# Kernel optimization log

Measured on AMD Instinct MI355X. Metric: run time of the kernel, lower is better.

Reference implementation:

```python
import jax, jax.numpy as jnp
import numpy as np

B, H, S, D = 2, 8, 2048, 64
N_HASHES = 6
EPS = 1e-8


def setup_inputs() -> dict:
    key = jax.random.key(0)
    kq, kk, kv, kr = jax.random.split(key, 4)
    Q = jax.random.normal(kq, (B, H, S, D), dtype=jnp.float32)
    K = jax.random.normal(kk, (B, H, S, D), dtype=jnp.float32)
    V = jax.random.normal(kv, (B, H, S, D), dtype=jnp.float32)
    rotations = jax.random.normal(kr, (H, N_HASHES, D), dtype=jnp.float32)
    return {"Q": Q, "K": K, "V": V, "rotations": rotations}


def _buckets(X, rotations, powers):
    # X: [b,h,l,d] -> integer bucket id per position, [b,h,l]
    Xn = X / (jnp.linalg.norm(X, axis=-1, keepdims=True) + 1e-8)
    bits = jnp.einsum('bhld,hnd->bhln', Xn, rotations) > 0
    return jnp.sum(bits.astype(jnp.int32) * powers, axis=-1)


def reference(Q, K, V, rotations):
    n_hashes = rotations.shape[1]
    d = Q.shape[-1]
    powers = (2 ** jnp.arange(n_hashes)).astype(jnp.int32)
    q_buckets = _buckets(Q, rotations, powers)  # [b,h,sq]
    k_buckets = _buckets(K, rotations, powers)  # [b,h,sk]
    # queries only attend to keys whose full hash code matches exactly
    match = q_buckets[..., :, None] == k_buckets[..., None, :]  # [b,h,sq,sk]
    scores = jnp.einsum('bhqd,bhkd->bhqk', Q, K) / (d ** 0.5)
    row_has = jnp.any(match, axis=-1, keepdims=True)
    masked = jnp.where(match, scores, -jnp.inf)
    m = jnp.max(masked, axis=-1, keepdims=True)
    m = jnp.where(row_has, m, 0.0)  # avoid -inf for empty rows
    e = jnp.where(match, jnp.exp(scores - m), 0.0)
    weights = e / (jnp.sum(e, axis=-1, keepdims=True) + EPS)
    out = jnp.einsum('bhqk,bhkd->bhqd', weights, V)
    return out / n_hashes
```

## Files before the change

kernel.cpp:

```cpp
#include <hip/hip_runtime.h>
#include <math.h>


constexpr int S_LEN = 2048;
constexpr int D = 64;
constexpr int NHASH = 6;
constexpr int BH = 16;
constexpr int NB = 64;
constexpr int QPAD = 4;
constexpr int PADQ = S_LEN + (QPAD - 1) * NB;
constexpr int NGRP = PADQ / QPAD;
constexpr int KCH = 32;

__global__ __launch_bounds__(256) void lsh_buckets2(const float* __restrict__ Q,
                                                    const float* __restrict__ K,
                                                    const float* __restrict__ rot,
                                                    int* __restrict__ qb,
                                                    int* __restrict__ kb) {
    const int gw   = (blockIdx.x * 256 + threadIdx.x) >> 6;
    const int lane = threadIdx.x & 63;
    const bool isK = gw >= BH * S_LEN;
    const int wid  = isK ? gw - BH * S_LEN : gw;
    const float* X = isK ? K : Q;
    int* dst       = isK ? kb : qb;
    const int h    = (wid >> 11) & 7;

    const float x  = X[(size_t)wid * D + lane];
    const float* r = rot + (size_t)h * NHASH * D + lane;
    float p0 = x * r[0 * D], p1 = x * r[1 * D], p2 = x * r[2 * D];
    float p3 = x * r[3 * D], p4 = x * r[4 * D], p5 = x * r[5 * D];
#pragma unroll
    for (int off = 32; off >= 1; off >>= 1) {
        p0 += __shfl_xor(p0, off, 64);
        p1 += __shfl_xor(p1, off, 64);
        p2 += __shfl_xor(p2, off, 64);
        p3 += __shfl_xor(p3, off, 64);
        p4 += __shfl_xor(p4, off, 64);
        p5 += __shfl_xor(p5, off, 64);
    }
    int bucket = (p0 > 0.f ? 1 : 0) | (p1 > 0.f ? 2 : 0) | (p2 > 0.f ? 4 : 0) |
                 (p3 > 0.f ? 8 : 0) | (p4 > 0.f ? 16 : 0) | (p5 > 0.f ? 32 : 0);
    if (lane == 0) dst[wid] = bucket;
}

__global__ __launch_bounds__(256) void lsh_build_desc(const int* __restrict__ qbuckets,
                                                      const int* __restrict__ kbuckets,
                                                      int* __restrict__ k_list,
                                                      int4* __restrict__ desc_q,
                                                      int* __restrict__ desc_k) {
    __shared__ unsigned short hist[256][NB + 1];
    __shared__ int base[NB + 1];
    __shared__ int seg[NB][4];
    __shared__ int qlist[PADQ];
    __shared__ int kcnt[NB], kst[NB];
    const int which = blockIdx.x >> 4;
    const int bh    = blockIdx.x & 15;
    const int tid   = threadIdx.x;
    const int* src  = (which ? kbuckets : qbuckets) + bh * S_LEN;

    for (int b = 0; b <= NB; ++b) hist[tid][b] = 0;
    if (!which) {
        for (int t = tid; t < PADQ; t += 256) qlist[t] = -1;
        if (tid < NB) kcnt[tid] = 0;
        __syncthreads();
        const int* kb = kbuckets + bh * S_LEN;
#pragma unroll
        for (int i = 0; i < 8; ++i)
            atomicAdd(&kcnt[kb[tid * 8 + i]], 1);
    }

    int myb[8];
#pragma unroll
    for (int i = 0; i < 8; ++i) {
        int b = src[tid * 8 + i];
        myb[i] = b;
        hist[tid][b]++;
    }
    __syncthreads();

    {
        const int b = tid >> 2, s = tid & 3;
        int sum = 0;
        for (int c = s * 64; c < s * 64 + 64; ++c) sum += hist[c][b];
        seg[b][s] = sum;
    }
    __syncthreads();
    if (tid < NB) {
        int run = 0;
#pragma unroll
        for (int s = 0; s < 4; ++s) {
            int t = seg[tid][s];
            seg[tid][s] = run;
            run += t;
        }
        base[tid] = run;
    }
    __syncthreads();

    if (tid == 0) {
        int run = 0;
        if (which) {
            for (int b = 0; b < NB; ++b) {
                int t = base[b];
                base[b] = run;
                run += t;
            }
        } else {
            for (int b = 0; b < NB; ++b) {
                int t = base[b];
                base[b] = run;
                run += (t + QPAD - 1) & ~(QPAD - 1);
            }
            int krun = 0;
            for (int b = 0; b < NB; ++b) {
                kst[b] = krun;
                krun += kcnt[b];
            }
        }
    }
    __syncthreads();

    {
        const int b = tid >> 2, s = tid & 3;
        int run = seg[b][s];
        for (int c = s * 64; c < s * 64 + 64; ++c) {
            int t = hist[c][b];
            hist[c][b] = (unsigned short)run;
            run += t;
        }
    }
    __syncthreads();

    if (which) {
        int* blist = k_list + bh * S_LEN;
#pragma unroll
        for (int i = 0; i < 8; ++i) {
            int b   = myb[i];
            int ofs = base[b] + hist[tid][b];
            hist[tid][b]++;
            blist[ofs] = tid * 8 + i;
        }
    } else {
#pragma unroll
        for (int i = 0; i < 8; ++i) {
            int b   = myb[i];
            int ofs = base[b] + hist[tid][b];
            hist[tid][b]++;
            qlist[ofs] = (tid * 8 + i) | (b << 16);
        }
        __syncthreads();
        for (int g = tid; g < NGRP; g += 256) {
            const int e0 = qlist[4 * g];
            int4 dq;
            int  dk = 0;
            if (e0 < 0) {
                dq = int4{-1, -1, -1, -1};
            } else {
                const int b  = e0 >> 16;
                const int e1 = qlist[4 * g + 1];
                const int e2 = qlist[4 * g + 2];
                const int e3 = qlist[4 * g + 3];
                dq.x = e0 & 0xFFFF;
                dq.y = e1 < 0 ? -1 : (e1 & 0xFFFF);
                dq.z = e2 < 0 ? -1 : (e2 & 0xFFFF);
                dq.w = e3 < 0 ? -1 : (e3 & 0xFFFF);
                dk   = kst[b] | (kcnt[b] << 16);
            }
            desc_q[bh * NGRP + g] = dq;
            desc_k[bh * NGRP + g] = dk;
        }
    }
}

__global__ __launch_bounds__(256) void lsh_attn_d(const float* __restrict__ Q,
                                                  const float* __restrict__ K,
                                                  const float* __restrict__ V,
                                                  const int4* __restrict__ desc_q,
                                                  const int* __restrict__ desc_k,
                                                  const int* __restrict__ k_list,
                                                  float* __restrict__ out) {
    __shared__ float qlds[4][QPAD][64];
    __shared__ float wbuf[4][QPAD][KCH];
    __shared__ int   kbuf[4][KCH];

    const int wv   = threadIdx.x >> 6;
    const int lane = threadIdx.x & 63;
    const int h    = lane >> 5;
    const int kk   = lane & 31;
    const int bh   = blockIdx.y;
    const int grp  = blockIdx.x * 4 + wv;

    const int4 dqv = desc_q[bh * NGRP + grp];
    const int q0 = __builtin_amdgcn_readfirstlane(dqv.x);
    if (q0 < 0) return;
    const int e1 = __builtin_amdgcn_readfirstlane(dqv.y);
    const int e2 = __builtin_amdgcn_readfirstlane(dqv.z);
    const int e3 = __builtin_amdgcn_readfirstlane(dqv.w);
    const int dk = __builtin_amdgcn_readfirstlane(desc_k[bh * NGRP + grp]);
    const int ks = dk & 0xFFFF;
    const int nk = dk >> 16;

    const bool v1 = e1 >= 0, v2 = e2 >= 0, v3 = e3 >= 0;
    const int q1 = v1 ? e1 : q0;
    const int q2 = v2 ? e2 : q0;
    const int q3 = v3 ? e3 : q0;

    float* outb = out + (size_t)bh * S_LEN * D;
    if (nk == 0) {
        outb[(size_t)q0 * D + lane] = 0.0f;
        if (v1) outb[(size_t)q1 * D + lane] = 0.0f;
        if (v2) outb[(size_t)q2 * D + lane] = 0.0f;
        if (v3) outb[(size_t)q3 * D + lane] = 0.0f;
        return;
    }

    const int* kl   = k_list + bh * S_LEN + ks;
    const float* Kb = K + (size_t)bh * S_LEN * D;
    const float* Vb = V + (size_t)bh * S_LEN * D;
    const float* Qb = Q + (size_t)bh * S_LEN * D;

    qlds[wv][0][lane] = Qb[(size_t)q0 * D + lane];
    qlds[wv][1][lane] = Qb[(size_t)q1 * D + lane];
    qlds[wv][2][lane] = Qb[(size_t)q2 * D + lane];
    qlds[wv][3][lane] = Qb[(size_t)q3 * D + lane];

    float l0 = 0.f, l1 = 0.f;
    float acc[QPAD] = {0.f, 0.f, 0.f, 0.f};

    for (int c = 0; c * KCH < nk; ++c) {
        const int cnk  = min(KCH, nk - c * KCH);
        const int kidx = kl[c * KCH + min(kk, cnk - 1)];
        const float* krow = Kb + (size_t)kidx * D + h * 32;

        float4 kv[8];
#pragma unroll
        for (int i = 0; i < 8; ++i) kv[i] = *(const float4*)(krow + i * 4);

        float s[QPAD];
#pragma unroll
        for (int j = 0; j < QPAD; ++j) {
            const float* qj = &qlds[wv][j][h * 32];
            float sj = 0.f;
#pragma unroll
            for (int i = 0; i < 8; ++i) {
                const float4 qv = *(const float4*)(qj + i * 4);
                sj += qv.x * kv[i].x + qv.y * kv[i].y + qv.z * kv[i].z + qv.w * kv[i].w;
            }
            s[j] = sj;
        }
        s[0] += __shfl_xor(s[0], 32, 64);
        s[1] += __shfl_xor(s[1], 32, 64);
        s[2] += __shfl_xor(s[2], 32, 64);
        s[3] += __shfl_xor(s[3], 32, 64);

        const bool kvalid = kk < cnk;
        const float sa = h ? s[2] : s[0];
        const float sb = h ? s[3] : s[1];
        const float ea = kvalid ? __expf(sa * 0.125f) : 0.f;
        const float eb = kvalid ? __expf(sb * 0.125f) : 0.f;
        l0 += ea;
        l1 += eb;
        wbuf[wv][2 * h + 0][kk] = ea;
        wbuf[wv][2 * h + 1][kk] = eb;
        if (h == 0) kbuf[wv][kk] = kidx;

        const int ng = (cnk + 3) >> 2;
        for (int g = 0; g < ng; ++g) {
            const int4 kx = *(const int4*)&kbuf[wv][g * 4];
            const float vx = Vb[(size_t)kx.x * D + lane];
            const float vy = Vb[(size_t)kx.y * D + lane];
            const float vz = Vb[(size_t)kx.z * D + lane];
            const float vw = Vb[(size_t)kx.w * D + lane];
            const float4 eA = *(const float4*)&wbuf[wv][0][g * 4];
            const float4 eB = *(const float4*)&wbuf[wv][1][g * 4];
            const float4 eC = *(const float4*)&wbuf[wv][2][g * 4];
            const float4 eD = *(const float4*)&wbuf[wv][3][g * 4];
            acc[0] += eA.x * vx + eA.y * vy + eA.z * vz + eA.w * vw;
            acc[1] += eB.x * vx + eB.y * vy + eB.z * vz + eB.w * vw;
            acc[2] += eC.x * vx + eC.y * vy + eC.z * vz + eC.w * vw;
            acc[3] += eD.x * vx + eD.y * vy + eD.z * vz + eD.w * vw;
        }
    }

#pragma unroll
    for (int off = 16; off >= 1; off >>= 1) {
        l0 += __shfl_xor(l0, off, 64);
        l1 += __shfl_xor(l1, off, 64);
    }
    const float o0 = __shfl_xor(l0, 32, 64);
    const float o1 = __shfl_xor(l1, 32, 64);
    const float lq0 = h ? o0 : l0;
    const float lq1 = h ? o1 : l1;
    const float lq2 = h ? l0 : o0;
    const float lq3 = h ? l1 : o1;

    const float inv6 = 1.0f / 6.0f;
    outb[(size_t)q0 * D + lane] = acc[0] / (lq0 + 1e-8f) * inv6;
    if (v1) outb[(size_t)q1 * D + lane] = acc[1] / (lq1 + 1e-8f) * inv6;
    if (v2) outb[(size_t)q2 * D + lane] = acc[2] / (lq2 + 1e-8f) * inv6;
    if (v3) outb[(size_t)q3 * D + lane] = acc[3] / (lq3 + 1e-8f) * inv6;
}

extern "C" void kernel_launch(void* const* d_in, const int* in_sizes, int n_in,
                              void* d_out, int out_size, void* d_ws, size_t ws_size,
                              hipStream_t stream) {
    const float* Q   = (const float*)d_in[0];
    const float* K   = (const float*)d_in[1];
    const float* V   = (const float*)d_in[2];
    const float* rot = (const float*)d_in[3];
    float* out = (float*)d_out;

    char* ws = (char*)d_ws;
    int* q_buckets = (int*)(ws);
    int* k_buckets = (int*)(ws + 131072);
    int* k_list    = (int*)(ws + 262144);
    int4* desc_q   = (int4*)(ws + 393216);
    int* desc_k    = (int*)(ws + 536576);

    lsh_buckets2<<<2 * BH * S_LEN / 4, 256, 0, stream>>>(Q, K, rot, q_buckets, k_buckets);
    lsh_build_desc<<<32, 256, 0, stream>>>(q_buckets, k_buckets, k_list, desc_q, desc_k);
    lsh_attn_d<<<dim3(NGRP / 4, BH), 256, 0, stream>>>(Q, K, V, desc_q, desc_k, k_list, out);
}
```

Before: 77.11 us.

## Split descriptor build into count-scan and atomic placement kernels

Replaces the 32-block build kernel, which ran serial per-bucket prefix scans and a large shared-memory histogram, with three steps. A small count/scan kernel uses a wave-level shfl scan, a memset pads the query list, and a grid-wide place kernel scatters indices with global atomics. The attention kernel now reads query groups straight from the padded list and looks up key ranges per bucket. It also interleaves waves across blocks, so each block mixes groups from different buckets. The cost is two extra launches, and the atomic placement makes in-bucket order nondeterministic.

New measurement: 83.46 us. +8.2%, slower.

```diff
diff --git a/kernel.cpp b/kernel.cpp
--- a/kernel.cpp
+++ b/kernel.cpp
@@ -10,6 +10,7 @@
 constexpr int QPAD = 4;
 constexpr int PADQ = S_LEN + (QPAD - 1) * NB;
 constexpr int NGRP = PADQ / QPAD;
+constexpr int NBLK = NGRP / 4;
 constexpr int KCH = 32;
 
 __global__ __launch_bounds__(256) void lsh_buckets2(const float* __restrict__ Q,
@@ -43,140 +44,70 @@
     if (lane == 0) dst[wid] = bucket;
 }
 
-__global__ __launch_bounds__(256) void lsh_build_desc(const int* __restrict__ qbuckets,
+__global__ __launch_bounds__(256) void lsh_count_scan(const int* __restrict__ qbuckets,
                                                       const int* __restrict__ kbuckets,
-                                                      int* __restrict__ k_list,
-                                                      int4* __restrict__ desc_q,
-                                                      int* __restrict__ desc_k) {
-    __shared__ unsigned short hist[256][NB + 1];
-    __shared__ int base[NB + 1];
-    __shared__ int seg[NB][4];
-    __shared__ int qlist[PADQ];
-    __shared__ int kcnt[NB], kst[NB];
+                                                      int* __restrict__ kstart_packed,
+                                                      int* __restrict__ cur_q,
+                                                      int* __restrict__ cur_k) {
+    __shared__ int hist[NB];
     const int which = blockIdx.x >> 4;
     const int bh    = blockIdx.x & 15;
     const int tid   = threadIdx.x;
     const int* src  = (which ? kbuckets : qbuckets) + bh * S_LEN;
 
-    for (int b = 0; b <= NB; ++b) hist[tid][b] = 0;
-    if (!which) {
-        for (int t = tid; t < PADQ; t += 256) qlist[t] = -1;
-        if (tid < NB) kcnt[tid] = 0;
-        __syncthreads();
-        const int* kb = kbuckets + bh * S_LEN;
-#pragma unroll
-        for (int i = 0; i < 8; ++i)
-            atomicAdd(&kcnt[kb[tid * 8 + i]], 1);
-    }
-
-    int myb[8];
-#pragma unroll
-    for (int i = 0; i < 8; ++i) {
-        int b = src[tid * 8 + i];
-        myb[i] = b;
-        hist[tid][b]++;
-    }
+    if (tid < NB) hist[tid] = 0;
     __syncthreads();
-
-    {
-        const int b = tid >> 2, s = tid & 3;
-        int sum = 0;
-        for (int c = s * 64; c < s * 64 + 64; ++c) sum += hist[c][b];
-        seg[b][s] = sum;
-    }
+#pragma unroll
+    for (int i = 0; i < 8; ++i)
+        atomicAdd(&hist[src[i * 256 + tid]], 1);
     __syncthreads();
-    if (tid < NB) {
-        int run = 0;
-#pragma unroll
-        for (int s = 0; s < 4; ++s) {
-            int t = seg[tid][s];
-            seg[tid][s] = run;
-            run += t;
-        }
-        base[tid] = run;
-    }
-    __syncthreads();
-
-    if (tid == 0) {
-        int run = 0;
+
+    if (tid < 64) {
+        const int cnt = hist[tid];
+        const int v   = which ? cnt : ((cnt + QPAD - 1) & ~(QPAD - 1));
+        int x = v;
+#pragma unroll
+        for (int off = 1; off < 64; off <<= 1) {
+            const int y = __shfl_up(x, off, 64);
+            if (tid >= off) x += y;
+        }
+        const int start = x - v;
         if (which) {
-            for (int b = 0; b < NB; ++b) {
-                int t = base[b];
-                base[b] = run;
-                run += t;
-            }
+            kstart_packed[bh * NB + tid] = start | (cnt << 16);
+            cur_k[bh * NB + tid] = start;
         } else {
-            for (int b = 0; b < NB; ++b) {
-                int t = base[b];
-                base[b] = run;
-                run += (t + QPAD - 1) & ~(QPAD - 1);
-            }
-            int krun = 0;
-            for (int b = 0; b < NB; ++b) {
-                kst[b] = krun;
-                krun += kcnt[b];
-            }
-        }
-    }
-    __syncthreads();
-
-    {
-        const int b = tid >> 2, s = tid & 3;
-        int run = seg[b][s];
-        for (int c = s * 64; c < s * 64 + 64; ++c) {
-            int t = hist[c][b];
-            hist[c][b] = (unsigned short)run;
-            run += t;
-        }
-    }
-    __syncthreads();
-
+            cur_q[bh * NB + tid] = start;
+        }
+    }
+}
+
+__global__ __launch_bounds__(256) void lsh_place(const int* __restrict__ qbuckets,
+                                                 const int* __restrict__ kbuckets,
+                                                 int* __restrict__ cur_q,
+                                                 int* __restrict__ cur_k,
+                                                 int* __restrict__ q_plist,
+                                                 int* __restrict__ k_list) {
+    const int gw    = blockIdx.x * 256 + threadIdx.x;
+    const int which = gw >> 15;
+    const int idx   = gw & (BH * S_LEN - 1);
+    const int bh    = idx >> 11;
+    const int i     = idx & (S_LEN - 1);
     if (which) {
-        int* blist = k_list + bh * S_LEN;
-#pragma unroll
-        for (int i = 0; i < 8; ++i) {
-            int b   = myb[i];
-            int ofs = base[b] + hist[tid][b];
-            hist[tid][b]++;
-            blist[ofs] = tid * 8 + i;
-        }
+        const int b    = kbuckets[idx];
+        const int slot = atomicAdd(&cur_k[bh * NB + b], 1);
+        k_list[bh * S_LEN + slot] = i;
     } else {
-#pragma unroll
-        for (int i = 0; i < 8; ++i) {
-            int b   = myb[i];
-            int ofs = base[b] + hist[tid][b];
-            hist[tid][b]++;
-            qlist[ofs] = (tid * 8 + i) | (b << 16);
-        }
-        __syncthreads();
-        for (int g = tid; g < NGRP; g += 256) {
-            const int e0 = qlist[4 * g];
-            int4 dq;
-            int  dk = 0;
-            if (e0 < 0) {
-                dq = int4{-1, -1, -1, -1};
-            } else {
-                const int b  = e0 >> 16;
-                const int e1 = qlist[4 * g + 1];
-                const int e2 = qlist[4 * g + 2];
-                const int e3 = qlist[4 * g + 3];
-                dq.x = e0 & 0xFFFF;
-                dq.y = e1 < 0 ? -1 : (e1 & 0xFFFF);
-                dq.z = e2 < 0 ? -1 : (e2 & 0xFFFF);
-                dq.w = e3 < 0 ? -1 : (e3 & 0xFFFF);
-                dk   = kst[b] | (kcnt[b] << 16);
-            }
-            desc_q[bh * NGRP + g] = dq;
-            desc_k[bh * NGRP + g] = dk;
-        }
+        const int b    = qbuckets[idx];
+        const int slot = atomicAdd(&cur_q[bh * NB + b], 1);
+        q_plist[bh * PADQ + slot] = i | (b << 16);
     }
 }
 
 __global__ __launch_bounds__(256) void lsh_attn_d(const float* __restrict__ Q,
                                                   const float* __restrict__ K,
                                                   const float* __restrict__ V,
-                                                  const int4* __restrict__ desc_q,
-                                                  const int* __restrict__ desc_k,
+                                                  const int* __restrict__ q_plist,
+                                                  const int* __restrict__ kstart_packed,
                                                   const int* __restrict__ k_list,
                                                   float* __restrict__ out) {
     __shared__ float qlds[4][QPAD][64];
@@ -188,22 +119,24 @@
     const int h    = lane >> 5;
     const int kk   = lane & 31;
     const int bh   = blockIdx.y;
-    const int grp  = blockIdx.x * 4 + wv;
-
-    const int4 dqv = desc_q[bh * NGRP + grp];
-    const int q0 = __builtin_amdgcn_readfirstlane(dqv.x);
-    if (q0 < 0) return;
+    const int grp  = blockIdx.x + wv * NBLK;
+
+    const int4 dqv = *(const int4*)(q_plist + bh * PADQ + 4 * grp);
+    const int e0 = __builtin_amdgcn_readfirstlane(dqv.x);
+    if (e0 < 0) return;
+    const int bucket = e0 >> 16;
     const int e1 = __builtin_amdgcn_readfirstlane(dqv.y);
     const int e2 = __builtin_amdgcn_readfirstlane(dqv.z);
     const int e3 = __builtin_amdgcn_readfirstlane(dqv.w);
-    const int dk = __builtin_amdgcn_readfirstlane(desc_k[bh * NGRP + grp]);
-    const int ks = dk & 0xFFFF;
-    const int nk = dk >> 16;
-
+    const int ksnk = __builtin_amdgcn_readfirstlane(kstart_packed[bh * NB + bucket]);
+    const int ks = ksnk & 0xFFFF;
+    const int nk = ksnk >> 16;
+
+    const int q0 = e0 & 0xFFFF;
     const bool v1 = e1 >= 0, v2 = e2 >= 0, v3 = e3 >= 0;
-    const int q1 = v1 ? e1 : q0;
-    const int q2 = v2 ? e2 : q0;
-    const int q3 = v3 ? e3 : q0;
+    const int q1 = v1 ? (e1 & 0xFFFF) : q0;
+    const int q2 = v2 ? (e2 & 0xFFFF) : q0;
+    const int q3 = v3 ? (e3 & 0xFFFF) : q0;
 
     float* outb = out + (size_t)bh * S_LEN * D;
     if (nk == 0) {
@@ -311,13 +244,19 @@
     float* out = (float*)d_out;
 
     char* ws = (char*)d_ws;
-    int* q_buckets = (int*)(ws);
-    int* k_buckets = (int*)(ws + 131072);
-    int* k_list    = (int*)(ws + 262144);
-    int4* desc_q   = (int4*)(ws + 393216);
-    int* desc_k    = (int*)(ws + 536576);
+    int* q_buckets     = (int*)(ws);
+    int* k_buckets     = (int*)(ws + 131072);
+    int* k_list        = (int*)(ws + 262144);
+    int* q_plist       = (int*)(ws + 393216);
+    int* kstart_packed = (int*)(ws + 540672);
+    int* cur_q         = (int*)(ws + 544768);
+    int* cur_k         = (int*)(ws + 548864);
 
     lsh_buckets2<<<2 * BH * S_LEN / 4, 256, 0, stream>>>(Q, K, rot, q_buckets, k_buckets);
-    lsh_build_desc<<<32, 256, 0, stream>>>(q_buckets, k_buckets, k_list, desc_q, desc_k);
-    lsh_attn_d<<<dim3(NGRP / 4, BH), 256, 0, stream>>>(Q, K, V, desc_q, desc_k, k_list, out);
-}
+    lsh_count_scan<<<32, 256, 0, stream>>>(q_buckets, k_buckets, kstart_packed, cur_q, cur_k);
+    hipMemsetAsync(q_plist, 0xFF, BH * PADQ * sizeof(int), stream);
+    lsh_place<<<2 * BH * S_LEN / 256, 256, 0, stream>>>(q_buckets, k_buckets, cur_q, cur_k,
+                                                        q_plist, k_list);
+    lsh_attn_d<<<dim3(NBLK, BH), 256, 0, stream>>>(Q, K, V, q_plist, kstart_packed,
+                                                   k_list, out);
+}
```
